# Kernel optimization log

Measured on AMD Instinct MI355X. Metric: run time of the kernel, lower is better.

The kernel has to match this reference:

```python
import jax, jax.numpy as jnp
import numpy as np

N_FEATURES = 512


def _hungarian(cost):
    """Jonker-Volgenant / e-maxx O(n^3) assignment on a square cost matrix.
    Host-side numpy, vectorized inner relaxation. Returns (row_ind, col_ind)
    matching scipy.optimize.linear_sum_assignment for square inputs."""
    n = cost.shape[0]
    INF = np.inf
    u = np.zeros(n + 1)
    v = np.zeros(n + 1)
    p = np.zeros(n + 1, dtype=np.int64)    # p[j] = row matched to column j (1-indexed)
    way = np.zeros(n + 1, dtype=np.int64)
    for i in range(1, n + 1):
        p[0] = i
        j0 = 0
        minv = np.full(n + 1, INF)
        used = np.zeros(n + 1, dtype=bool)
        while True:
            used[j0] = True
            i0 = p[j0]
            free = ~used
            free[0] = False
            cols = np.nonzero(free)[0]
            cur = cost[i0 - 1, cols - 1] - u[i0] - v[cols]
            improve = cur < minv[cols]
            minv[cols] = np.where(improve, cur, minv[cols])
            way[cols] = np.where(improve, j0, way[cols])
            k = int(np.argmin(minv[cols]))
            delta = minv[cols][k]
            j1 = int(cols[k])
            u[p[used]] += delta
            v[used] -= delta
            minv[free] -= delta
            j0 = j1
            if p[j0] == 0:
                break
        while j0:
            j1 = way[j0]
            p[j0] = p[j1]
            j0 = j1
    col_of_row = np.empty(n, dtype=np.int64)
    col_of_row[p[1:] - 1] = np.arange(n)
    return np.arange(n), col_of_row


def setup_inputs() -> dict:
    key = jax.random.key(0)
    k1, k2, k3, k4 = jax.random.split(key, 4)
    n = N_FEATURES
    # Learned diagram parameter, built as in ToFU.__init__ with birth_lims=(0,1), birth_death=True
    b = jax.random.uniform(k1, (n,), dtype=jnp.float32)
    d = b + jax.random.uniform(k2, (n,), dtype=jnp.float32)
    dgm = jnp.stack([b, d], axis=1)            # [n, 2]
    # Target diagram from the data pipeline
    bx = jax.random.uniform(k3, (n,), dtype=jnp.float32)
    dx = bx + jax.random.uniform(k4, (n,), dtype=jnp.float32)
    dgm_x = jnp.stack([bx, dx], axis=1)        # [n, 2]
    return {"dgm": dgm, "dgm_x": dgm_x}


def reference(dgm, dgm_x):
    # --- host-side combinatorial matching (mirrors detach().cpu().numpy() + scipy) ---
    dgm_np = np.asarray(dgm, dtype=np.float64)
    x_np = np.asarray(dgm_x, dtype=np.float64)
    # cdist, euclidean metric: [n, m]
    cost = np.sqrt(((dgm_np[:, None, :] - x_np[None, :, :]) ** 2).sum(-1))
    tofu_idx, target_idx = _hungarian(cost)
    ti = jnp.asarray(tofu_idx)
    ci = jnp.asarray(target_idx)
    # --- differentiable loss (indices are constants; dgm_target rows come from dgm_x) ---
    dgm_target = jax.lax.stop_gradient(dgm).at[ti].set(dgm_x[ci])
    return 0.5 * ((dgm - dgm_target) ** 2).sum()
```

## Files before the change

kernel.cpp:

```cpp
#include <hip/hip_runtime.h>
#include <cfloat>
#include <math.h>

#define N 512
typedef unsigned long long u64_t;

__device__ __forceinline__ u64_t map_f64(double x) {
    u64_t b = (u64_t)__double_as_longlong(x);
    return b ^ ((b >> 63) ? 0xFFFFFFFFFFFFFFFFull : 0x8000000000000000ull);
}
__device__ __forceinline__ double unmap_f64(u64_t b) {
    b ^= ((b >> 63) ? 0x8000000000000000ull : 0xFFFFFFFFFFFFFFFFull);
    return __longlong_as_double((long long)b);
}

__device__ __forceinline__ u64_t wave_min_key(u64_t key) {
    unsigned hi = (unsigned)(key >> 32), lo = (unsigned)key;
#define MIN_STAGE(CTRL)                                                        \
    {                                                                          \
        unsigned oh = (unsigned)__builtin_amdgcn_update_dpp((int)hi, (int)hi,  \
                                                            CTRL, 0xF, 0xF, false); \
        unsigned ol = (unsigned)__builtin_amdgcn_update_dpp((int)lo, (int)lo,  \
                                                            CTRL, 0xF, 0xF, false); \
        const u64_t o = ((u64_t)oh << 32) | ol;                                \
        const u64_t c = ((u64_t)hi << 32) | lo;                                \
        if (o < c) { hi = oh; lo = ol; }                                       \
    }
    MIN_STAGE(0x111) MIN_STAGE(0x112) MIN_STAGE(0x114) MIN_STAGE(0x118)
    MIN_STAGE(0x142) MIN_STAGE(0x143)
#undef MIN_STAGE
    return ((u64_t)hi << 32) | lo;
}

__global__ __launch_bounds__(512, 1) void tofu_solver(
    const float* __restrict__ dgm, const float* __restrict__ dgm_x,
    float* __restrict__ out)
{
#pragma clang fp contract(off)
    __shared__ double2 pt[N];
    __shared__ double  u_lds[N + 1];
    __shared__ int     p_lds[N + 1];
    __shared__ int     way_lds[N + 1];
    __shared__ int     claim[N + 1];
    __shared__ int     flist[4 * N + 32];
    __shared__ u64_t   dslot[3];
    __shared__ u64_t   aslot[2], bslot[2];
    __shared__ double  v1x;
    __shared__ double  red8[8];
    __shared__ int     nfree_s;

    const int tid  = threadIdx.x;
    const int col  = tid + 1;
    const int lane = tid & 63;
    const int wid  = tid >> 6;
    const float2* dgm2  = (const float2*)dgm;
    const float2* dgmx2 = (const float2*)dgm_x;

    {
        const float2 p2 = dgm2[tid];
        pt[tid] = make_double2((double)p2.x, (double)p2.y);
    }
    const float2 q2 = dgmx2[tid];
    const double xb = (double)q2.x, xd = (double)q2.y;
    u_lds[col] = 0.0; p_lds[col] = 0; way_lds[col] = 0; claim[col] = 0x7fffffff;
    if (tid == 0) {
        u_lds[0] = 0.0; p_lds[0] = 0; way_lds[0] = 0; claim[0] = 0x7fffffff;
        dslot[0] = dslot[1] = dslot[2] = ~0ull;
        aslot[0] = aslot[1] = ~0ull; bslot[0] = bslot[1] = ~0ull;
    }
    __syncthreads();

    double v_j; int amin;
    {
        double vsq = DBL_MAX; amin = 1;
        for (int i = 0; i < N; ++i) {
            const double2 rp = pt[i];
            const double db = rp.x - xb, dd = rp.y - xd;
            const double sq = db * db + dd * dd;
            if (sq < vsq) { vsq = sq; amin = i + 1; }
        }
        v_j = sqrt(vsq);
    }

    atomicMin(&claim[amin], col);
    __syncthreads();
    if (claim[amin] == col) p_lds[col] = amin;
    __syncthreads();
    claim[col] = 0;
    __syncthreads();
    { const int r = p_lds[col]; if (r) claim[r] = 1; }
    __syncthreads();
    if (tid == 0) {
        int nf = 0;
        for (int r = 1; r <= N; ++r) if (!claim[r]) flist[nf++] = r;
        nfree_s = nf;
    }
    __syncthreads();

    {
        int head = 0, tail = nfree_s, q = 0;
        const int cap = 3 * tail + 16;
        int myp = p_lds[col];
        for (int step = 0; step < cap && head < tail; ++step) {
            const int i = flist[head++];
            const double2 rp = pt[i - 1];
            const double db = rp.x - xb, dd = rp.y - xd;
            const double val = sqrt(db * db + dd * dd) - v_j;
            const u64_t key = (map_f64(val) & ~0x7FFFFull)
                            | ((u64_t)(col - 1) << 10) | (u64_t)myp;
            u64_t kr = wave_min_key(key);
            if (lane == 63) atomicMin(&aslot[q], kr);
            __syncthreads();
            const u64_t k1 = aslot[q];
            const int j1    = (int)((k1 >> 10) & 511) + 1;
            const int k_old = (int)(k1 & 1023);
            if (col == j1) v1x = val;
            kr = wave_min_key((col == j1) ? ~0ull : key);
            if (lane == 63) atomicMin(&bslot[q], kr);
            __syncthreads();
            const double m2t = unmap_f64(bslot[q] & ~0x7FFFFull);
            const double v1e = v1x;
            const double ui  = fmax(m2t, v1e);
            if (col == j1) { v_j -= (ui - val); myp = i; }
            if (tid == 0) {
                u_lds[i] = ui;
                p_lds[j1] = i;
                if (k_old) flist[tail] = k_old;
                aslot[q ^ 1] = ~0ull; bslot[q ^ 1] = ~0ull;
            }
            if (k_old) ++tail;
            q ^= 1;
            __syncthreads();
        }
    }

    claim[col] = 0;
    __syncthreads();
    { const int r = p_lds[col]; if (r) claim[r] = 1; }
    __syncthreads();
    if (tid == 0) {
        int nf = 0;
        for (int r = 1; r <= N; ++r) if (!claim[r]) flist[nf++] = r;
        nfree_s = nf;
    }
    __syncthreads();
    const int nfree = nfree_s;

    for (int kk = 0; kk < nfree; ++kk) {
        const int iroot = flist[kk];
        const int pcol  = p_lds[col];
        if (tid == 0) p_lds[0] = iroot;
        double minv = DBL_MAX, du = 0.0, du0 = 0.0;
        bool used = false;
        int juse = 0, i0 = iroot, par = 0;

        while (true) {
            if (col == juse) used = true;
            const double2 rp = pt[i0 - 1];
            const double u0 = u_lds[i0];
            u64_t key = ~0ull;
            if (!used) {
                const double db = rp.x - xb, dd = rp.y - xd;
                const double c = sqrt(db * db + dd * dd);
                const double cur = (c - u0) - v_j;
                if (cur < minv) { minv = cur; way_lds[col] = juse; }
                key = (map_f64(minv) & ~0x7FFFFull)
                    | ((u64_t)(col - 1) << 10) | (u64_t)pcol;
            }
            key = wave_min_key(key);
            if (lane == 63) atomicMin(&dslot[par], key);
            __syncthreads();
            const u64_t k = dslot[par];
            if (tid == 0) dslot[(par + 2) % 3] = ~0ull;
            const double delta = unmap_f64(k & ~0x7FFFFull);
            if (used) { v_j -= delta; du += delta; }
            else        minv -= delta;
            if (tid == 0) du0 += delta;
            juse = (int)((k >> 10) & 511) + 1;
            i0   = (int)(k & 1023);
            if (i0 == 0) break;
            par = (par + 1) % 3;
        }

        if (used) u_lds[pcol] += du;
        if (tid == 0) {
            u_lds[iroot] += du0;
            dslot[par] = ~0ull;
            int j = juse;
            while (j) { const int jn = way_lds[j]; p_lds[j] = p_lds[jn]; j = jn; }
        }
        __syncthreads();
    }

    const int r = p_lds[col] - 1;
    const float2 a = dgm2[r];
    const float2 b = dgmx2[tid];
    const float fb = a.x - b.x;
    const float fd = a.y - b.y;
    double acc = (double)fb * (double)fb + (double)fd * (double)fd;
    #pragma unroll
    for (int m = 32; m >= 1; m >>= 1) acc += __shfl_xor(acc, m, 64);
    if (lane == 0) red8[wid] = acc;
    __syncthreads();
    if (tid == 0) {
        double s = 0.0;
        #pragma unroll
        for (int w = 0; w < 8; ++w) s += red8[w];
        out[0] = (float)(0.5 * s);
    }
}

extern "C" void kernel_launch(void* const* d_in, const int* in_sizes, int n_in,
                              void* d_out, int out_size, void* d_ws, size_t ws_size,
                              hipStream_t stream) {
    const float* dgm   = (const float*)d_in[0];
    const float* dgm_x = (const float*)d_in[1];
    float* out = (float*)d_out;
    tofu_solver<<<1, 512, 0, stream>>>(dgm, dgm_x, out);
}
```

Measured before the change: 5.769 ms.

## Halve block to 256 threads with two columns each and per-wave reduction slots

The single-block Hungarian solver now runs 256 threads, each owning two columns, so the block has 4 waves instead of 8. The cross-wave minimum no longer uses LDS atomicMin into a shared slot that must be reset. Each wave writes its own slot and every thread takes the minimum of the 4 slots, which removes the atomics and slot-reset bookkeeping. The aim is to cut the cost of each barrier-bound, latency-dominated Dijkstra step, in exchange for twice the per-thread arithmetic per step.

Result: slower. 6.306 ms (+9.3%).

```diff
diff --git a/kernel.cpp b/kernel.cpp
--- a/kernel.cpp
+++ b/kernel.cpp
@@ -32,7 +32,14 @@
     return ((u64_t)hi << 32) | lo;
 }
 
-__global__ __launch_bounds__(512, 1) void tofu_solver(
+__device__ __forceinline__ u64_t min4_u64(const u64_t* s) {
+    const u64_t a = s[0], b = s[1], c = s[2], d = s[3];
+    const u64_t m0 = (a < b) ? a : b;
+    const u64_t m1 = (c < d) ? c : d;
+    return (m0 < m1) ? m0 : m1;
+}
+
+__global__ __launch_bounds__(256, 1) void tofu_solver(
     const float* __restrict__ dgm, const float* __restrict__ dgm_x,
     float* __restrict__ out)
 {
@@ -43,52 +50,63 @@
     __shared__ int     way_lds[N + 1];
     __shared__ int     claim[N + 1];
     __shared__ int     flist[4 * N + 32];
-    __shared__ u64_t   dslot[3];
-    __shared__ u64_t   aslot[2], bslot[2];
+    __shared__ u64_t   dslot[2][4];
+    __shared__ u64_t   aslot[2][4], bslot[2][4];
     __shared__ double  v1x;
-    __shared__ double  red8[8];
+    __shared__ double  red4[4];
     __shared__ int     nfree_s;
 
     const int tid  = threadIdx.x;
-    const int col  = tid + 1;
+    const int col0 = tid + 1;
+    const int col1 = tid + 257;
     const int lane = tid & 63;
     const int wid  = tid >> 6;
     const float2* dgm2  = (const float2*)dgm;
     const float2* dgmx2 = (const float2*)dgm_x;
 
     {
-        const float2 p2 = dgm2[tid];
+        float2 p2 = dgm2[tid];
         pt[tid] = make_double2((double)p2.x, (double)p2.y);
-    }
-    const float2 q2 = dgmx2[tid];
-    const double xb = (double)q2.x, xd = (double)q2.y;
-    u_lds[col] = 0.0; p_lds[col] = 0; way_lds[col] = 0; claim[col] = 0x7fffffff;
+        p2 = dgm2[tid + 256];
+        pt[tid + 256] = make_double2((double)p2.x, (double)p2.y);
+    }
+    const float2 qa = dgmx2[tid];
+    const float2 qb = dgmx2[tid + 256];
+    const double xb0 = (double)qa.x, xd0 = (double)qa.y;
+    const double xb1 = (double)qb.x, xd1 = (double)qb.y;
+    u_lds[col0] = 0.0; p_lds[col0] = 0; way_lds[col0] = 0; claim[col0] = 0x7fffffff;
+    u_lds[col1] = 0.0; p_lds[col1] = 0; way_lds[col1] = 0; claim[col1] = 0x7fffffff;
     if (tid == 0) {
         u_lds[0] = 0.0; p_lds[0] = 0; way_lds[0] = 0; claim[0] = 0x7fffffff;
-        dslot[0] = dslot[1] = dslot[2] = ~0ull;
-        aslot[0] = aslot[1] = ~0ull; bslot[0] = bslot[1] = ~0ull;
-    }
-    __syncthreads();
-
-    double v_j; int amin;
+    }
+    __syncthreads();
+
+    double v_j0, v_j1; int amin0, amin1;
     {
-        double vsq = DBL_MAX; amin = 1;
+        double vsq0 = DBL_MAX, vsq1 = DBL_MAX; amin0 = 1; amin1 = 1;
         for (int i = 0; i < N; ++i) {
             const double2 rp = pt[i];
-            const double db = rp.x - xb, dd = rp.y - xd;
-            const double sq = db * db + dd * dd;
-            if (sq < vsq) { vsq = sq; amin = i + 1; }
-        }
-        v_j = sqrt(vsq);
-    }
-
-    atomicMin(&claim[amin], col);
-    __syncthreads();
-    if (claim[amin] == col) p_lds[col] = amin;
-    __syncthreads();
-    claim[col] = 0;
-    __syncthreads();
-    { const int r = p_lds[col]; if (r) claim[r] = 1; }
+            const double db0 = rp.x - xb0, dd0 = rp.y - xd0;
+            const double db1 = rp.x - xb1, dd1 = rp.y - xd1;
+            const double sq0 = db0 * db0 + dd0 * dd0;
+            const double sq1 = db1 * db1 + dd1 * dd1;
+            if (sq0 < vsq0) { vsq0 = sq0; amin0 = i + 1; }
+            if (sq1 < vsq1) { vsq1 = sq1; amin1 = i + 1; }
+        }
+        v_j0 = sqrt(vsq0);
+        v_j1 = sqrt(vsq1);
+    }
+
+    atomicMin(&claim[amin0], col0);
+    atomicMin(&claim[amin1], col1);
+    __syncthreads();
+    if (claim[amin0] == col0) p_lds[col0] = amin0;
+    if (claim[amin1] == col1) p_lds[col1] = amin1;
+    __syncthreads();
+    claim[col0] = 0; claim[col1] = 0;
+    __syncthreads();
+    { const int r = p_lds[col0]; if (r) claim[r] = 1; }
+    { const int r = p_lds[col1]; if (r) claim[r] = 1; }
     __syncthreads();
     if (tid == 0) {
         int nf = 0;
@@ -100,33 +118,40 @@
     {
         int head = 0, tail = nfree_s, q = 0;
         const int cap = 3 * tail + 16;
-        int myp = p_lds[col];
+        int myp0 = p_lds[col0], myp1 = p_lds[col1];
         for (int step = 0; step < cap && head < tail; ++step) {
             const int i = flist[head++];
             const double2 rp = pt[i - 1];
-            const double db = rp.x - xb, dd = rp.y - xd;
-            const double val = sqrt(db * db + dd * dd) - v_j;
-            const u64_t key = (map_f64(val) & ~0x7FFFFull)
-                            | ((u64_t)(col - 1) << 10) | (u64_t)myp;
-            u64_t kr = wave_min_key(key);
-            if (lane == 63) atomicMin(&aslot[q], kr);
-            __syncthreads();
-            const u64_t k1 = aslot[q];
+            const double db0 = rp.x - xb0, dd0 = rp.y - xd0;
+            const double db1 = rp.x - xb1, dd1 = rp.y - xd1;
+            const double val0 = sqrt(db0 * db0 + dd0 * dd0) - v_j0;
+            const double val1 = sqrt(db1 * db1 + dd1 * dd1) - v_j1;
+            const u64_t key0 = (map_f64(val0) & ~0x7FFFFull)
+                             | ((u64_t)(col0 - 1) << 10) | (u64_t)myp0;
+            const u64_t key1 = (map_f64(val1) & ~0x7FFFFull)
+                             | ((u64_t)(col1 - 1) << 10) | (u64_t)myp1;
+            u64_t kr = wave_min_key((key0 < key1) ? key0 : key1);
+            if (lane == 63) aslot[q][wid] = kr;
+            __syncthreads();
+            const u64_t k1 = min4_u64(aslot[q]);
             const int j1    = (int)((k1 >> 10) & 511) + 1;
             const int k_old = (int)(k1 & 1023);
-            if (col == j1) v1x = val;
-            kr = wave_min_key((col == j1) ? ~0ull : key);
-            if (lane == 63) atomicMin(&bslot[q], kr);
-            __syncthreads();
-            const double m2t = unmap_f64(bslot[q] & ~0x7FFFFull);
+            if (col0 == j1) v1x = val0;
+            if (col1 == j1) v1x = val1;
+            const u64_t e0 = (col0 == j1) ? ~0ull : key0;
+            const u64_t e1 = (col1 == j1) ? ~0ull : key1;
+            kr = wave_min_key((e0 < e1) ? e0 : e1);
+            if (lane == 63) bslot[q][wid] = kr;
+            __syncthreads();
+            const double m2t = unmap_f64(min4_u64(bslot[q]) & ~0x7FFFFull);
             const double v1e = v1x;
             const double ui  = fmax(m2t, v1e);
-            if (col == j1) { v_j -= (ui - val); myp = i; }
+            if (col0 == j1) { v_j0 -= (ui - val0); myp0 = i; }
+            if (col1 == j1) { v_j1 -= (ui - val1); myp1 = i; }
             if (tid == 0) {
                 u_lds[i] = ui;
                 p_lds[j1] = i;
                 if (k_old) flist[tail] = k_old;
-                aslot[q ^ 1] = ~0ull; bslot[q ^ 1] = ~0ull;
             }
             if (k_old) ++tail;
             q ^= 1;
@@ -134,9 +159,10 @@
         }
     }
 
-    claim[col] = 0;
-    __syncthreads();
-    { const int r = p_lds[col]; if (r) claim[r] = 1; }
+    claim[col0] = 0; claim[col1] = 0;
+    __syncthreads();
+    { const int r = p_lds[col0]; if (r) claim[r] = 1; }
+    { const int r = p_lds[col1]; if (r) claim[r] = 1; }
     __syncthreads();
     if (tid == 0) {
         int nf = 0;
@@ -148,65 +174,77 @@
 
     for (int kk = 0; kk < nfree; ++kk) {
         const int iroot = flist[kk];
-        const int pcol  = p_lds[col];
+        const int pcol0 = p_lds[col0];
+        const int pcol1 = p_lds[col1];
         if (tid == 0) p_lds[0] = iroot;
-        double minv = DBL_MAX, du = 0.0, du0 = 0.0;
-        bool used = false;
+        double minv0 = DBL_MAX, minv1 = DBL_MAX;
+        double duA = 0.0, duB = 0.0, du0 = 0.0;
+        bool used0 = false, used1 = false;
         int juse = 0, i0 = iroot, par = 0;
 
         while (true) {
-            if (col == juse) used = true;
+            if (col0 == juse) used0 = true;
+            if (col1 == juse) used1 = true;
             const double2 rp = pt[i0 - 1];
             const double u0 = u_lds[i0];
             u64_t key = ~0ull;
-            if (!used) {
-                const double db = rp.x - xb, dd = rp.y - xd;
+            if (!used0) {
+                const double db = rp.x - xb0, dd = rp.y - xd0;
                 const double c = sqrt(db * db + dd * dd);
-                const double cur = (c - u0) - v_j;
-                if (cur < minv) { minv = cur; way_lds[col] = juse; }
-                key = (map_f64(minv) & ~0x7FFFFull)
-                    | ((u64_t)(col - 1) << 10) | (u64_t)pcol;
+                const double cur = (c - u0) - v_j0;
+                if (cur < minv0) { minv0 = cur; way_lds[col0] = juse; }
+                key = (map_f64(minv0) & ~0x7FFFFull)
+                    | ((u64_t)(col0 - 1) << 10) | (u64_t)pcol0;
+            }
+            if (!used1) {
+                const double db = rp.x - xb1, dd = rp.y - xd1;
+                const double c = sqrt(db * db + dd * dd);
+                const double cur = (c - u0) - v_j1;
+                if (cur < minv1) { minv1 = cur; way_lds[col1] = juse; }
+                const u64_t k1 = (map_f64(minv1) & ~0x7FFFFull)
+                               | ((u64_t)(col1 - 1) << 10) | (u64_t)pcol1;
+                if (k1 < key) key = k1;
             }
             key = wave_min_key(key);
-            if (lane == 63) atomicMin(&dslot[par], key);
-            __syncthreads();
-            const u64_t k = dslot[par];
-            if (tid == 0) dslot[(par + 2) % 3] = ~0ull;
+            if (lane == 63) dslot[par][wid] = key;
+            __syncthreads();
+            const u64_t k = min4_u64(dslot[par]);
             const double delta = unmap_f64(k & ~0x7FFFFull);
-            if (used) { v_j -= delta; du += delta; }
-            else        minv -= delta;
+            if (used0) { v_j0 -= delta; duA += delta; } else minv0 -= delta;
+            if (used1) { v_j1 -= delta; duB += delta; } else minv1 -= delta;
             if (tid == 0) du0 += delta;
             juse = (int)((k >> 10) & 511) + 1;
             i0   = (int)(k & 1023);
             if (i0 == 0) break;
-            par = (par + 1) % 3;
-        }
-
-        if (used) u_lds[pcol] += du;
+            par ^= 1;
+        }
+
+        if (used0) u_lds[pcol0] += duA;
+        if (used1) u_lds[pcol1] += duB;
         if (tid == 0) {
             u_lds[iroot] += du0;
-            dslot[par] = ~0ull;
             int j = juse;
             while (j) { const int jn = way_lds[j]; p_lds[j] = p_lds[jn]; j = jn; }
         }
         __syncthreads();
     }
 
-    const int r = p_lds[col] - 1;
-    const float2 a = dgm2[r];
-    const float2 b = dgmx2[tid];
-    const float fb = a.x - b.x;
-    const float fd = a.y - b.y;
-    double acc = (double)fb * (double)fb + (double)fd * (double)fd;
+    const int r0 = p_lds[col0] - 1;
+    const int r1 = p_lds[col1] - 1;
+    const float2 a0 = dgm2[r0];
+    const float2 b0 = dgmx2[tid];
+    const float2 a1 = dgm2[r1];
+    const float2 b1 = dgmx2[tid + 256];
+    const float fb0 = a0.x - b0.x, fd0 = a0.y - b0.y;
+    const float fb1 = a1.x - b1.x, fd1 = a1.y - b1.y;
+    double acc = (double)fb0 * (double)fb0 + (double)fd0 * (double)fd0
+               + (double)fb1 * (double)fb1 + (double)fd1 * (double)fd1;
     #pragma unroll
     for (int m = 32; m >= 1; m >>= 1) acc += __shfl_xor(acc, m, 64);
-    if (lane == 0) red8[wid] = acc;
-    __syncthreads();
-    if (tid == 0) {
-        double s = 0.0;
-        #pragma unroll
-        for (int w = 0; w < 8; ++w) s += red8[w];
-        out[0] = (float)(0.5 * s);
+    if (lane == 0) red4[wid] = acc;
+    __syncthreads();
+    if (tid == 0) {
+        out[0] = (float)(0.5 * (red4[0] + red4[1] + red4[2] + red4[3]));
     }
 }
 
@@ -216,5 +254,5 @@
     const float* dgm   = (const float*)d_in[0];
     const float* dgm_x = (const float*)d_in[1];
     float* out = (float*)d_out;
-    tofu_solver<<<1, 512, 0, stream>>>(dgm, dgm_x, out);
-}
+    tofu_solver<<<1, 256, 0, stream>>>(dgm, dgm_x, out);
+}
```

## Use cumulative dual offsets and skip redundant wave reductions in augmenting loop

Applied to the files above, without the earlier changes.

The per-iteration delta updates to minv, v_j and u are replaced by a cumulative offset D, with minv stored in absolute terms so it never has to be rewritten each step. Dual corrections are applied once, after the augmenting path is found. A squared-distance pruning test skips the sqrt when a column cannot improve. The wave-level min reduction runs only when some lane's key changed, and otherwise the cached wave minimum is reused. This cuts per-step arithmetic and DPP shuffles on the serial critical path, at the cost of accumulated floating-point drift and an epsilon-based pruning test that could change tie-breaking.

After: 5.641 ms, median of 3. -2.2%, faster.

```diff
diff --git a/kernel.cpp b/kernel.cpp
--- a/kernel.cpp
+++ b/kernel.cpp
@@ -150,41 +150,57 @@
         const int iroot = flist[kk];
         const int pcol  = p_lds[col];
         if (tid == 0) p_lds[0] = iroot;
-        double minv = DBL_MAX, du = 0.0, du0 = 0.0;
+        double minv = DBL_MAX;
+        double D = 0.0, Dwin = 0.0;
         bool used = false;
         int juse = 0, i0 = iroot, par = 0;
+        u64_t key  = ~0ull;
+        u64_t wmin = ~0ull;
 
         while (true) {
-            if (col == juse) used = true;
+            bool trans = false;
+            if (col == juse) {
+                used = true; Dwin = D; trans = true; key = ~0ull;
+            }
             const double2 rp = pt[i0 - 1];
             const double u0 = u_lds[i0];
-            u64_t key = ~0ull;
+            bool upd = false;
             if (!used) {
                 const double db = rp.x - xb, dd = rp.y - xd;
-                const double c = sqrt(db * db + dd * dd);
-                const double cur = (c - u0) - v_j;
-                if (cur < minv) { minv = cur; way_lds[col] = juse; }
-                key = (map_f64(minv) & ~0x7FFFFull)
-                    | ((u64_t)(col - 1) << 10) | (u64_t)pcol;
-            }
-            key = wave_min_key(key);
-            if (lane == 63) atomicMin(&dslot[par], key);
+                const double s = db * db + dd * dd;
+                const double T  = ((minv - D) + u0) + v_j;
+                const double Tp = T + 1e-12;
+                if (Tp > 0.0 && s < Tp * Tp) {
+                    const double c = sqrt(s);
+                    const double cand = D + ((c - u0) - v_j);
+                    if (cand < minv) {
+                        minv = cand; way_lds[col] = juse; upd = true;
+                        key = (map_f64(minv) & ~0x7FFFFull)
+                            | ((u64_t)(col - 1) << 10) | (u64_t)pcol;
+                    }
+                }
+            }
+            if (__any((int)(upd || trans))) {
+                wmin = wave_min_key(key);
+            }
+            if (lane == 63) atomicMin(&dslot[par], wmin);
             __syncthreads();
             const u64_t k = dslot[par];
             if (tid == 0) dslot[(par + 2) % 3] = ~0ull;
-            const double delta = unmap_f64(k & ~0x7FFFFull);
-            if (used) { v_j -= delta; du += delta; }
-            else        minv -= delta;
-            if (tid == 0) du0 += delta;
+            D = unmap_f64(k & ~0x7FFFFull);
             juse = (int)((k >> 10) & 511) + 1;
             i0   = (int)(k & 1023);
             if (i0 == 0) break;
             par = (par + 1) % 3;
         }
 
-        if (used) u_lds[pcol] += du;
+        if (used) {
+            const double du = D - Dwin;
+            u_lds[pcol] += du;
+            v_j -= du;
+        }
         if (tid == 0) {
-            u_lds[iroot] += du0;
+            u_lds[iroot] += D;
             dslot[par] = ~0ull;
             int j = juse;
             while (j) { const int jn = way_lds[j]; p_lds[j] = p_lds[jn]; j = jn; }
```

## Run augmenting-path search in a single wavefront with lazy dual offsets

Applied to the files above, without the earlier changes.

Moves the Hungarian augmentation phase from 512 threads with block-wide barriers per step onto one 64-lane wavefront, each lane handling 8 columns in registers. Instead of subtracting delta from every minv each step, it keeps a running offset D and applies dual updates once per augmentation. It adds a float-precision prefilter that skips the double sqrt when a candidate cannot beat the current minimum. This removes __syncthreads and LDS atomics from the inner loop, but cuts parallelism per step by 8x and relies on the float margin being large enough to keep results identical.

Measured after the change: 13.16 ms. 2.28x slower.

```diff
diff --git a/kernel.cpp b/kernel.cpp
--- a/kernel.cpp
+++ b/kernel.cpp
@@ -38,12 +38,14 @@
 {
 #pragma clang fp contract(off)
     __shared__ double2 pt[N];
+    __shared__ float2  ptf[N];
     __shared__ double  u_lds[N + 1];
+    __shared__ float   uf[N + 1];
+    __shared__ double  vj_lds[N + 1];
     __shared__ int     p_lds[N + 1];
     __shared__ int     way_lds[N + 1];
     __shared__ int     claim[N + 1];
     __shared__ int     flist[4 * N + 32];
-    __shared__ u64_t   dslot[3];
     __shared__ u64_t   aslot[2], bslot[2];
     __shared__ double  v1x;
     __shared__ double  red8[8];
@@ -58,14 +60,14 @@
 
     {
         const float2 p2 = dgm2[tid];
-        pt[tid] = make_double2((double)p2.x, (double)p2.y);
+        pt[tid]  = make_double2((double)p2.x, (double)p2.y);
+        ptf[tid] = p2;
     }
     const float2 q2 = dgmx2[tid];
     const double xb = (double)q2.x, xd = (double)q2.y;
     u_lds[col] = 0.0; p_lds[col] = 0; way_lds[col] = 0; claim[col] = 0x7fffffff;
     if (tid == 0) {
         u_lds[0] = 0.0; p_lds[0] = 0; way_lds[0] = 0; claim[0] = 0x7fffffff;
-        dslot[0] = dslot[1] = dslot[2] = ~0ull;
         aslot[0] = aslot[1] = ~0ull; bslot[0] = bslot[1] = ~0ull;
     }
     __syncthreads();
@@ -143,54 +145,107 @@
         for (int r = 1; r <= N; ++r) if (!claim[r]) flist[nf++] = r;
         nfree_s = nf;
     }
+    vj_lds[col] = v_j;
+    uf[col] = (float)u_lds[col];
+    if (tid == 0) uf[0] = 0.0f;
     __syncthreads();
     const int nfree = nfree_s;
 
-    for (int kk = 0; kk < nfree; ++kk) {
-        const int iroot = flist[kk];
-        const int pcol  = p_lds[col];
-        if (tid == 0) p_lds[0] = iroot;
-        double minv = DBL_MAX, du = 0.0, du0 = 0.0;
-        bool used = false;
-        int juse = 0, i0 = iroot, par = 0;
-
-        while (true) {
-            if (col == juse) used = true;
-            const double2 rp = pt[i0 - 1];
-            const double u0 = u_lds[i0];
-            u64_t key = ~0ull;
-            if (!used) {
-                const double db = rp.x - xb, dd = rp.y - xd;
-                const double c = sqrt(db * db + dd * dd);
-                const double cur = (c - u0) - v_j;
-                if (cur < minv) { minv = cur; way_lds[col] = juse; }
-                key = (map_f64(minv) & ~0x7FFFFull)
-                    | ((u64_t)(col - 1) << 10) | (u64_t)pcol;
-            }
-            key = wave_min_key(key);
-            if (lane == 63) atomicMin(&dslot[par], key);
-            __syncthreads();
-            const u64_t k = dslot[par];
-            if (tid == 0) dslot[(par + 2) % 3] = ~0ull;
-            const double delta = unmap_f64(k & ~0x7FFFFull);
-            if (used) { v_j -= delta; du += delta; }
-            else        minv -= delta;
-            if (tid == 0) du0 += delta;
-            juse = (int)((k >> 10) & 511) + 1;
-            i0   = (int)(k & 1023);
-            if (i0 == 0) break;
-            par = (par + 1) % 3;
-        }
-
-        if (used) u_lds[pcol] += du;
-        if (tid == 0) {
-            u_lds[iroot] += du0;
-            dslot[par] = ~0ull;
-            int j = juse;
-            while (j) { const int jn = way_lds[j]; p_lds[j] = p_lds[jn]; j = jn; }
-        }
-        __syncthreads();
-    }
+    if (wid == 0) {
+        double xbk[8], xdk[8], vj[8];
+        float  xbf[8], xdf[8], vjf[8];
+        #pragma unroll
+        for (int k = 0; k < 8; ++k) {
+            const int c = (k << 6) + lane;
+            const float2 q = dgmx2[c];
+            xbf[k] = q.x;          xdf[k] = q.y;
+            xbk[k] = (double)q.x;  xdk[k] = (double)q.y;
+            vj[k]  = vj_lds[c + 1];
+            vjf[k] = (float)vj[k];
+        }
+
+        for (int kk = 0; kk < nfree; ++kk) {
+            const int iroot = flist[kk];
+            if (lane == 0) p_lds[0] = iroot;
+            int    pcol[8];
+            double minv[8], Dwin[8];
+            float  mf[8];
+            u64_t  key[8];
+            unsigned usedm = 0;
+            #pragma unroll
+            for (int k = 0; k < 8; ++k) {
+                pcol[k] = p_lds[(k << 6) + lane + 1];
+                minv[k] = DBL_MAX;
+                mf[k]   = (float)DBL_MAX;
+                Dwin[k] = 0.0;
+                key[k]  = ~0ull;
+            }
+            double D = 0.0;
+            int juse = 0, i0 = iroot;
+
+            while (true) {
+                #pragma unroll
+                for (int k = 0; k < 8; ++k) {
+                    if (((k << 6) + lane + 1) == juse) {
+                        usedm |= (1u << k); Dwin[k] = D; key[k] = ~0ull;
+                    }
+                }
+                const double2 rp  = pt[i0 - 1];
+                const float2  rpf = ptf[i0 - 1];
+                const double  u0  = u_lds[i0];
+                const float   uf0 = uf[i0];
+                const float   Df  = (float)D;
+                #pragma unroll
+                for (int k = 0; k < 8; ++k) {
+                    if (!(usedm & (1u << k))) {
+                        const float dbf = rpf.x - xbf[k], ddf = rpf.y - xdf[k];
+                        const float sf  = dbf * dbf + ddf * ddf;
+                        const float Tpf = ((mf[k] - Df) + uf0) + vjf[k] + 1e-4f;
+                        if (Tpf > 0.0f && sf < Tpf * Tpf) {
+                            const double db = rp.x - xbk[k], dd = rp.y - xdk[k];
+                            const double c = sqrt(db * db + dd * dd);
+                            const double cand = D + ((c - u0) - vj[k]);
+                            if (cand < minv[k]) {
+                                minv[k] = cand; mf[k] = (float)cand;
+                                way_lds[(k << 6) + lane + 1] = juse;
+                                key[k] = (map_f64(cand) & ~0x7FFFFull)
+                                       | ((u64_t)((k << 6) + lane) << 10)
+                                       | (u64_t)pcol[k];
+                            }
+                        }
+                    }
+                }
+                u64_t lkey = key[0];
+                #pragma unroll
+                for (int k = 1; k < 8; ++k) lkey = (key[k] < lkey) ? key[k] : lkey;
+                const u64_t wmin = wave_min_key(lkey);
+                const unsigned whi = (unsigned)__builtin_amdgcn_readlane((int)(unsigned)(wmin >> 32), 63);
+                const unsigned wlo = (unsigned)__builtin_amdgcn_readlane((int)(unsigned)wmin, 63);
+                const u64_t kwin = ((u64_t)whi << 32) | wlo;
+                D    = unmap_f64(kwin & ~0x7FFFFull);
+                juse = (int)((kwin >> 10) & 511) + 1;
+                i0   = (int)(kwin & 1023);
+                if (i0 == 0) break;
+            }
+
+            #pragma unroll
+            for (int k = 0; k < 8; ++k) {
+                if (usedm & (1u << k)) {
+                    const double du = D - Dwin[k];
+                    const double nu = u_lds[pcol[k]] + du;
+                    u_lds[pcol[k]] = nu; uf[pcol[k]] = (float)nu;
+                    vj[k] -= du; vjf[k] = (float)vj[k];
+                }
+            }
+            if (lane == 0) {
+                const double nu = u_lds[iroot] + D;
+                u_lds[iroot] = nu; uf[iroot] = (float)nu;
+                int j = juse;
+                while (j) { const int jn = way_lds[j]; p_lds[j] = p_lds[jn]; j = jn; }
+            }
+        }
+    }
+    __syncthreads();
 
     const int r = p_lds[col] - 1;
     const float2 a = dgm2[r];
```
